# Performance work log

Hardware: AMD Instinct MI355X
Metric: run time of the kernel (lower is better)

## Reference

```python
import jax, jax.numpy as jnp
import numpy as np

N_NODES = 50000
N_EDGES = 800000
IN_CH, HID_CH, OUT_CH = 512, 128, 64


def gcn_conv(x, W, b, src, dst, num_nodes):
    """PyG GCNConv: add self-loops, sym-normalize, linear, scatter-add, bias.
    x: [N, Fin], W: [Fout, Fin], b: [Fout], src/dst: [E] int."""
    loop = jnp.arange(num_nodes, dtype=src.dtype)
    src2 = jnp.concatenate([src, loop])  # [E+N]
    dst2 = jnp.concatenate([dst, loop])
    deg = jax.ops.segment_sum(jnp.ones_like(dst2, dtype=x.dtype), dst2,
                              num_segments=num_nodes)  # in-degree + 1
    d_inv_sqrt = jnp.where(deg > 0, jax.lax.rsqrt(deg), 0.0)
    norm = d_inv_sqrt[src2] * d_inv_sqrt[dst2]  # [E+N]
    h = x @ W.T  # [N, Fout]
    msg = h[src2] * norm[:, None]  # [E+N, Fout] -- dominant memory traffic
    out = jax.ops.segment_sum(msg, dst2, num_segments=num_nodes)
    return out + b


def setup_inputs() -> dict:
    key = jax.random.key(0)
    ks = jax.random.split(key, 8)
    x = jax.random.normal(ks[0], (N_NODES, IN_CH), dtype=jnp.float32)
    edge_index = jax.random.randint(ks[1], (2, N_EDGES), 0, N_NODES, dtype=jnp.int64)
    s1 = 1.0 / np.sqrt(IN_CH)
    s2 = 1.0 / np.sqrt(HID_CH)
    W1 = jax.random.normal(ks[2], (HID_CH, IN_CH), dtype=jnp.float32) * s1
    b1 = jnp.zeros((HID_CH,), dtype=jnp.float32)
    W_mu = jax.random.normal(ks[3], (OUT_CH, HID_CH), dtype=jnp.float32) * s2
    b_mu = jnp.zeros((OUT_CH,), dtype=jnp.float32)
    W_logstd = jax.random.normal(ks[4], (OUT_CH, HID_CH), dtype=jnp.float32) * s2
    b_logstd = jnp.zeros((OUT_CH,), dtype=jnp.float32)
    return {"x": x, "edge_index": edge_index, "W1": W1, "b1": b1,
            "W_mu": W_mu, "b_mu": b_mu, "W_logstd": W_logstd, "b_logstd": b_logstd}


def reference(x, edge_index, W1, b1, W_mu, b_mu, W_logstd, b_logstd):
    src, dst = edge_index[0], edge_index[1]
    n = x.shape[0]
    h = jax.nn.relu(gcn_conv(x, W1, b1, src, dst, n))
    mu = gcn_conv(h, W_mu, b_mu, src, dst, n)
    logstd = gcn_conv(h, W_logstd, b_logstd, src, dst, n)
    return (mu, logstd)
```

## Files before the change

### kernel.cpp

```cpp
#include <hip/hip_runtime.h>

constexpr int FIN = 512;
constexpr int FH  = 128;
constexpr int FO  = 64;

typedef short short8 __attribute__((ext_vector_type(8)));
typedef float f32x4 __attribute__((ext_vector_type(4)));

__device__ __forceinline__ unsigned short f2bf(float f) {
    unsigned u = __float_as_uint(f);
    u += 0x7fffu + ((u >> 16) & 1u);
    return (unsigned short)(u >> 16);
}
__device__ __forceinline__ float bf2f(unsigned short h) {
    return __uint_as_float((unsigned)h << 16);
}
__device__ __forceinline__ float bflo(unsigned v) { return __uint_as_float(v << 16); }
__device__ __forceinline__ float bfhi(unsigned v) { return __uint_as_float(v & 0xffff0000u); }


__global__ void pre_kernel(const int* __restrict__ dst, int* __restrict__ cnt, int E,
                           const float* __restrict__ W1, unsigned short* __restrict__ W1b,
                           const float* __restrict__ Wmu, const float* __restrict__ Wlg,
                           unsigned short* __restrict__ Wh, unsigned short* __restrict__ Wl,
                           int cntB) {
    int b = blockIdx.x;
    if (b < cntB) {
        int i = b * 256 + threadIdx.x;
        if (i < E) atomicAdd(&cnt[dst[i]], 1);
    } else if (b < cntB + 64) {
        int i = (b - cntB) * 256 + threadIdx.x;
        float4 v = ((const float4*)W1)[i];
        ushort4 p;
        p.x = f2bf(v.x); p.y = f2bf(v.y); p.z = f2bf(v.z); p.w = f2bf(v.w);
        ((ushort4*)W1b)[i] = p;
    } else {
        int i = (b - cntB - 64) * 256 + threadIdx.x;
        int r = i >> 7, c = i & 127;
        float f = (r < 64) ? Wmu[r * 128 + c] : Wlg[(r - 64) * 128 + c];
        unsigned short h = f2bf(f);
        Wh[i] = h;
        Wl[i] = f2bf(f - bf2f(h));
    }
}


__global__ void scan1_kernel(const int* __restrict__ cnt, int* __restrict__ offs,
                             int* __restrict__ bsum, float* __restrict__ dinv, int n) {
    __shared__ int sdata[256];
    int t = threadIdx.x;
    int base = blockIdx.x * 1024 + t * 4;
    int4 c = make_int4(0, 0, 0, 0);
    if (base + 3 < n) {
        c = *(const int4*)(cnt + base);
    } else {
        if (base + 0 < n) c.x = cnt[base + 0];
        if (base + 1 < n) c.y = cnt[base + 1];
        if (base + 2 < n) c.z = cnt[base + 2];
        if (base + 3 < n) c.w = cnt[base + 3];
    }
    if (base + 0 < n) dinv[base + 0] = rsqrtf((float)(c.x + 1));
    if (base + 1 < n) dinv[base + 1] = rsqrtf((float)(c.y + 1));
    if (base + 2 < n) dinv[base + 2] = rsqrtf((float)(c.z + 1));
    if (base + 3 < n) dinv[base + 3] = rsqrtf((float)(c.w + 1));

    int s0 = c.x + c.y + c.z + c.w;
    sdata[t] = s0;
    __syncthreads();
    for (int off = 1; off < 256; off <<= 1) {
        int v = (t >= off) ? sdata[t - off] : 0;
        __syncthreads();
        sdata[t] += v;
        __syncthreads();
    }
    int excl = sdata[t] - s0;
    if (t == 255) bsum[blockIdx.x] = sdata[255];
    if (base + 0 < n) offs[base + 0] = excl;
    if (base + 1 < n) offs[base + 1] = excl + c.x;
    if (base + 2 < n) offs[base + 2] = excl + c.x + c.y;
    if (base + 3 < n) offs[base + 3] = excl + c.x + c.y + c.z;
}

__global__ void scan2_kernel(int* __restrict__ bsum, int nb) {
    __shared__ int sdata[256];
    int t = threadIdx.x;
    int v = (t < nb) ? bsum[t] : 0;
    sdata[t] = v;
    __syncthreads();
    for (int off = 1; off < 256; off <<= 1) {
        int u = (t >= off) ? sdata[t - off] : 0;
        __syncthreads();
        sdata[t] += u;
        __syncthreads();
    }
    if (t < nb) bsum[t] = sdata[t] - v;
}

__global__ void scan3_kernel(int* __restrict__ offs, const int* __restrict__ bsum,
                             int n, int E) {
    int i = blockIdx.x * blockDim.x + threadIdx.x;
    if (i < n) offs[i] += bsum[i >> 10];
    if (i == 0) offs[n] = E;
}


__global__ void fill_kernel(const int* __restrict__ src, const int* __restrict__ dst,
                            const float* __restrict__ dinv, const int* __restrict__ offs,
                            int* __restrict__ cursor, int2* __restrict__ esort, int E) {
    int i = blockIdx.x * blockDim.x + threadIdx.x;
    if (i < E) {
        int s = src[i];
        int d = dst[i];
        int pos = offs[d] + atomicAdd(&cursor[d], 1);
        float w = dinv[s] * dinv[d];
        esort[pos] = make_int2(s, __float_as_int(w));
    }
}


__global__ void spmm_kernel(const unsigned int* __restrict__ hin, const int* __restrict__ offs,
                            const int2* __restrict__ esort, const float* __restrict__ dinv,
                            const float* __restrict__ bias, unsigned int* __restrict__ hout,
                            int n, int relu) {
    int gid = blockIdx.x * blockDim.x + threadIdx.x;
    int node = gid >> 6;
    int lane = threadIdx.x & 63;
    if (node >= n) return;
    float di = dinv[node];
    unsigned hv = hin[(size_t)node * 64 + lane];
    float ax = di * di * bflo(hv);
    float ay = di * di * bfhi(hv);
    int p = offs[node];
    int end = offs[node + 1];
    if ((p & 1) && p < end) {
        int2 e = esort[p];
        unsigned v = hin[(size_t)e.x * 64 + lane];
        float w = __int_as_float(e.y);
        ax = fmaf(w, bflo(v), ax); ay = fmaf(w, bfhi(v), ay);
        ++p;
    }
    for (; p + 8 <= end; p += 8) {
        int4 q0 = *(const int4*)(esort + p + 0);
        int4 q1 = *(const int4*)(esort + p + 2);
        int4 q2 = *(const int4*)(esort + p + 4);
        int4 q3 = *(const int4*)(esort + p + 6);
        unsigned v0 = hin[(size_t)q0.x * 64 + lane];
        unsigned v1 = hin[(size_t)q0.z * 64 + lane];
        unsigned v2 = hin[(size_t)q1.x * 64 + lane];
        unsigned v3 = hin[(size_t)q1.z * 64 + lane];
        unsigned v4 = hin[(size_t)q2.x * 64 + lane];
        unsigned v5 = hin[(size_t)q2.z * 64 + lane];
        unsigned v6 = hin[(size_t)q3.x * 64 + lane];
        unsigned v7 = hin[(size_t)q3.z * 64 + lane];
        float w0 = __int_as_float(q0.y), w1 = __int_as_float(q0.w);
        float w2 = __int_as_float(q1.y), w3 = __int_as_float(q1.w);
        float w4 = __int_as_float(q2.y), w5 = __int_as_float(q2.w);
        float w6 = __int_as_float(q3.y), w7 = __int_as_float(q3.w);
        ax = fmaf(w0, bflo(v0), ax); ay = fmaf(w0, bfhi(v0), ay);
        ax = fmaf(w1, bflo(v1), ax); ay = fmaf(w1, bfhi(v1), ay);
        ax = fmaf(w2, bflo(v2), ax); ay = fmaf(w2, bfhi(v2), ay);
        ax = fmaf(w3, bflo(v3), ax); ay = fmaf(w3, bfhi(v3), ay);
        ax = fmaf(w4, bflo(v4), ax); ay = fmaf(w4, bfhi(v4), ay);
        ax = fmaf(w5, bflo(v5), ax); ay = fmaf(w5, bfhi(v5), ay);
        ax = fmaf(w6, bflo(v6), ax); ay = fmaf(w6, bfhi(v6), ay);
        ax = fmaf(w7, bflo(v7), ax); ay = fmaf(w7, bfhi(v7), ay);
    }
    for (; p + 2 <= end; p += 2) {
        int4 q = *(const int4*)(esort + p);
        unsigned v0 = hin[(size_t)q.x * 64 + lane];
        unsigned v1 = hin[(size_t)q.z * 64 + lane];
        float w0 = __int_as_float(q.y), w1 = __int_as_float(q.w);
        ax = fmaf(w0, bflo(v0), ax); ay = fmaf(w0, bfhi(v0), ay);
        ax = fmaf(w1, bflo(v1), ax); ay = fmaf(w1, bfhi(v1), ay);
    }
    if (p < end) {
        int2 e = esort[p];
        unsigned v = hin[(size_t)e.x * 64 + lane];
        float w = __int_as_float(e.y);
        ax = fmaf(w, bflo(v), ax); ay = fmaf(w, bfhi(v), ay);
    }
    if (bias) {
        float2 b = ((const float2*)bias)[lane];
        ax += b.x; ay += b.y;
    }
    if (relu) { ax = fmaxf(ax, 0.f); ay = fmaxf(ay, 0.f); }
    unsigned o = (unsigned)f2bf(ax) | ((unsigned)f2bf(ay) << 16);
    hout[(size_t)node * 64 + lane] = o;
}


__global__ __launch_bounds__(1024, 4) void gemm1_kernel(
    const float* __restrict__ X, const unsigned short* __restrict__ Wb,
    unsigned short* __restrict__ out, int M, int nstrips) {
    extern __shared__ __align__(16) unsigned short Bs[];
    int tid = threadIdx.x;

    #pragma unroll
    for (int j = 0; j < 8; ++j) {
        int f = tid + j * 1024;
        int row = f >> 6;
        unsigned addr = ((unsigned)f << 4) ^ ((unsigned)(row & 7) << 4);
        *(short8*)((char*)Bs + addr) = ((const short8*)Wb)[f];
    }
    __syncthreads();

    int lane = tid & 63, wid = tid >> 6;
    int fr = lane & 15, fq = lane >> 4;
    int s = wid * gridDim.x + blockIdx.x;
    if (s >= nstrips) return;
    int row0 = s * 16;
    int arow = row0 + fr; if (arow >= M) arow = M - 1;
    const float* ap = X + (size_t)arow * FIN + fq * 8;

    f32x4 acc[8] = {};

    float4 c0 = *(const float4*)(ap + 0);
    float4 c1 = *(const float4*)(ap + 4);
    float4 c2 = *(const float4*)(ap + 32);
    float4 c3 = *(const float4*)(ap + 36);

    #pragma unroll
    for (int kk = 0; kk < 8; ++kk) {
        int k0 = kk * 64;
        float4 d0 = c0, d1 = c1, d2 = c2, d3 = c3;
        if (kk < 7) {
            c0 = *(const float4*)(ap + k0 + 64);
            c1 = *(const float4*)(ap + k0 + 68);
            c2 = *(const float4*)(ap + k0 + 96);
            c3 = *(const float4*)(ap + k0 + 100);
        }
        short8 af0, af1;
        af0[0] = (short)f2bf(d0.x); af0[1] = (short)f2bf(d0.y);
        af0[2] = (short)f2bf(d0.z); af0[3] = (short)f2bf(d0.w);
        af0[4] = (short)f2bf(d1.x); af0[5] = (short)f2bf(d1.y);
        af0[6] = (short)f2bf(d1.z); af0[7] = (short)f2bf(d1.w);
        af1[0] = (short)f2bf(d2.x); af1[1] = (short)f2bf(d2.y);
        af1[2] = (short)f2bf(d2.z); af1[3] = (short)f2bf(d2.w);
        af1[4] = (short)f2bf(d3.x); af1[5] = (short)f2bf(d3.y);
        af1[6] = (short)f2bf(d3.z); af1[7] = (short)f2bf(d3.w);

        int cb0 = k0 * 2 + fq * 16;
        #pragma unroll
        for (int c = 0; c < 8; ++c) {
            int br = c * 16 + fr;
            short8 b0 = *(const short8*)((const char*)Bs + br * 1024 +
                                         ((unsigned)cb0 ^ ((unsigned)(br & 7) << 4)));
            acc[c] = __builtin_amdgcn_mfma_f32_16x16x32_bf16(af0, b0, acc[c], 0, 0, 0);
        }
        int cb1 = cb0 + 64;
        #pragma unroll
        for (int c = 0; c < 8; ++c) {
            int br = c * 16 + fr;
            short8 b1 = *(const short8*)((const char*)Bs + br * 1024 +
                                         ((unsigned)cb1 ^ ((unsigned)(br & 7) << 4)));
            acc[c] = __builtin_amdgcn_mfma_f32_16x16x32_bf16(af1, b1, acc[c], 0, 0, 0);
        }
    }

    #pragma unroll
    for (int c = 0; c < 8; ++c) {
        #pragma unroll
        for (int j = 0; j < 4; ++j) {
            int row = row0 + fq * 4 + j;
            if (row < M) out[(size_t)row * FH + c * 16 + fr] = f2bf(acc[c][j]);
        }
    }
}


__global__ __launch_bounds__(512) void gemm2_kernel(
    const unsigned short* __restrict__ Xb,
    const unsigned short* __restrict__ Wh, const unsigned short* __restrict__ Wl,
    float* __restrict__ outA, float* __restrict__ outB,
    const float* __restrict__ biasA, const float* __restrict__ biasB,
    int M, int nstrips) {
    __shared__ __align__(16) unsigned short WhS[128 * 128];
    __shared__ __align__(16) unsigned short WlS[128 * 128];
    int tid = threadIdx.x;

    #pragma unroll
    for (int j = 0; j < 4; ++j) {
        int f = tid + j * 512;
        int row = f >> 4;
        unsigned addr = ((unsigned)f * 16u) ^ ((unsigned)(row & 7) << 4);
        *(short8*)((char*)WhS + addr) = ((const short8*)Wh)[f];
        *(short8*)((char*)WlS + addr) = ((const short8*)Wl)[f];
    }
    __syncthreads();

    int lane = tid & 63, wid = tid >> 6;
    int fr = lane & 15, fq = lane >> 4;
    int s = blockIdx.x * 8 + wid;
    if (s >= nstrips) return;
    int row0 = s * 16;
    int arow = row0 + fr; if (arow > M - 1) arow = M - 1;
    const unsigned short* ap = Xb + (size_t)arow * FH + fq * 8;

    short8 a0 = *(const short8*)(ap + 0);
    short8 a1 = *(const short8*)(ap + 32);
    short8 a2 = *(const short8*)(ap + 64);
    short8 a3 = *(const short8*)(ap + 96);

    f32x4 acc[8] = {};

    auto proc = [&](int k0, short8 a) {
        int cb = k0 * 2 + fq * 16;
        #pragma unroll
        for (int c = 0; c < 8; ++c) {
            int lr = c * 16 + fr;
            unsigned addr = ((unsigned)(lr * 256 + cb)) ^ ((unsigned)(lr & 7) << 4);
            short8 bh = *(const short8*)((const char*)WhS + addr);
            short8 bl = *(const short8*)((const char*)WlS + addr);
            acc[c] = __builtin_amdgcn_mfma_f32_16x16x32_bf16(a, bh, acc[c], 0, 0, 0);
            acc[c] = __builtin_amdgcn_mfma_f32_16x16x32_bf16(a, bl, acc[c], 0, 0, 0);
        }
    };
    proc(0, a0);
    proc(32, a1);
    proc(64, a2);
    proc(96, a3);

    #pragma unroll
    for (int c = 0; c < 8; ++c) {
        float* outp = (c < 4) ? outA : outB;
        const float* bp = (c < 4) ? biasA : biasB;
        int col = (c & 3) * 16 + fr;
        float bv = bp[col];
        #pragma unroll
        for (int j = 0; j < 4; ++j) {
            int row = row0 + fq * 4 + j;
            if (row < M) outp[(size_t)row * FO + col] = acc[c][j] + bv;
        }
    }
}


extern "C" void kernel_launch(void* const* d_in, const int* in_sizes, int n_in,
                              void* d_out, int out_size, void* d_ws, size_t ws_size,
                              hipStream_t stream) {
    const float* x   = (const float*)d_in[0];
    const int*   ei  = (const int*)d_in[1];
    const float* W1  = (const float*)d_in[2];
    const float* b1  = (const float*)d_in[3];
    const float* Wmu = (const float*)d_in[4];
    const float* bmu = (const float*)d_in[5];
    const float* Wlg = (const float*)d_in[6];
    const float* blg = (const float*)d_in[7];

    const int n = in_sizes[0] / FIN;
    const int E = in_sizes[1] / 2;
    const int* src = ei;
    const int* dst = ei + E;
    const int nstrips = (n + 15) / 16;

    char* ws = (char*)d_ws;
    size_t off = 0;
    auto alloc = [&](size_t bytes) -> void* {
        void* p = ws + off;
        off = (off + bytes + 255) & ~((size_t)255);
        return p;
    };
    int*   cnt    = (int*)  alloc((size_t)n * 4);
    int*   offs   = (int*)  alloc((size_t)(n + 1) * 4);
    int*   cursor = (int*)  alloc((size_t)n * 4);
    int*   bsum   = (int*)  alloc(1024);
    float* dinv   = (float*)alloc((size_t)n * 4);
    int2*  esort  = (int2*) alloc((size_t)E * 8);
    unsigned short* hbf  = (unsigned short*)alloc((size_t)n * FH * 2);
    unsigned short* h1bf = (unsigned short*)alloc((size_t)n * FH * 2);
    unsigned short* ah2b = (unsigned short*)alloc((size_t)n * FH * 2);
    unsigned short* W1b = (unsigned short*)alloc((size_t)FH * FIN * 2);
    unsigned short* W2h = (unsigned short*)alloc((size_t)FH * FH * 2);
    unsigned short* W2l = (unsigned short*)alloc((size_t)FH * FH * 2);

    hipMemsetAsync(cnt, 0, (size_t)n * 4, stream);
    hipMemsetAsync(cursor, 0, (size_t)n * 4, stream);

    int cntB = (E + 255) / 256;
    pre_kernel<<<cntB + 128, 256, 0, stream>>>(dst, cnt, E, W1, W1b, Wmu, Wlg, W2h, W2l, cntB);

    int nb = (n + 1023) / 1024;
    scan1_kernel<<<nb, 256, 0, stream>>>(cnt, offs, bsum, dinv, n);
    scan2_kernel<<<1, 256, 0, stream>>>(bsum, nb);
    scan3_kernel<<<(n + 255) / 256, 256, 0, stream>>>(offs, bsum, n, E);

    fill_kernel<<<(E + 255) / 256, 256, 0, stream>>>(src, dst, dinv, offs, cursor, esort, E);

    gemm1_kernel<<<256, 1024, 128 * 1024, stream>>>(x, W1b, hbf, n, nstrips);
    spmm_kernel<<<(n + 3) / 4, 256, 0, stream>>>(
        (const unsigned*)hbf, offs, esort, dinv, b1, (unsigned*)h1bf, n, 1);
    spmm_kernel<<<(n + 3) / 4, 256, 0, stream>>>(
        (const unsigned*)h1bf, offs, esort, dinv, nullptr, (unsigned*)ah2b, n, 0);
    float* outmu = (float*)d_out;
    float* outlg = outmu + (size_t)n * FO;
    gemm2_kernel<<<(nstrips + 7) / 8, 512, 0, stream>>>(
        ah2b, W2h, W2l, outmu, outlg, bmu, blg, n, nstrips);
}
```

Baseline: 197.0 us.

## Split SpMM feature columns across blocks and process four edges per wavefront

The SpMM kernel is restructured so each wavefront covers one node but only a 16-column quarter of its features. The four 16-lane groups each take a different edge, and partial sums are combined with cross-lane shuffles. Blocks are ordered so the four column-quarter blocks for the same node group run adjacently, which should keep gathered rows and the edge list hot in cache. This gives more parallelism and memory requests in flight per edge, at the cost of reading the edge list four times and giving up the wider unrolled int4 loads of the old loop.

```diff
diff --git a/kernel.cpp b/kernel.cpp
--- a/kernel.cpp
+++ b/kernel.cpp
@@ -122,70 +122,44 @@
                             const int2* __restrict__ esort, const float* __restrict__ dinv,
                             const float* __restrict__ bias, unsigned int* __restrict__ hout,
                             int n, int relu) {
-    int gid = blockIdx.x * blockDim.x + threadIdx.x;
-    int node = gid >> 6;
+    int blk = blockIdx.x;
+    int r = blk & 7;
+    int g = blk >> 3;
+    int q = r & 3;
+    int ngrp = g * 2 + (r >> 2);
+    int wid = threadIdx.x >> 6;
+    int node = ngrp * 4 + wid;
+    if (node >= n) return;
     int lane = threadIdx.x & 63;
-    if (node >= n) return;
-    float di = dinv[node];
-    unsigned hv = hin[(size_t)node * 64 + lane];
-    float ax = di * di * bflo(hv);
-    float ay = di * di * bfhi(hv);
-    int p = offs[node];
-    int end = offs[node + 1];
-    if ((p & 1) && p < end) {
-        int2 e = esort[p];
-        unsigned v = hin[(size_t)e.x * 64 + lane];
+    int eslot = lane >> 4, cl = lane & 15;
+    const unsigned* hq = hin + q * 16 + cl;
+
+    int p0 = offs[node], end = offs[node + 1];
+    float ax = 0.f, ay = 0.f;
+    for (int p = p0; p < end; p += 4) {
+        int pe = p + eslot;
+        int2 e = (pe < end) ? esort[pe] : make_int2(node, 0);
+        unsigned v = hq[(size_t)e.x * 64];
         float w = __int_as_float(e.y);
-        ax = fmaf(w, bflo(v), ax); ay = fmaf(w, bfhi(v), ay);
-        ++p;
-    }
-    for (; p + 8 <= end; p += 8) {
-        int4 q0 = *(const int4*)(esort + p + 0);
-        int4 q1 = *(const int4*)(esort + p + 2);
-        int4 q2 = *(const int4*)(esort + p + 4);
-        int4 q3 = *(const int4*)(esort + p + 6);
-        unsigned v0 = hin[(size_t)q0.x * 64 + lane];
-        unsigned v1 = hin[(size_t)q0.z * 64 + lane];
-        unsigned v2 = hin[(size_t)q1.x * 64 + lane];
-        unsigned v3 = hin[(size_t)q1.z * 64 + lane];
-        unsigned v4 = hin[(size_t)q2.x * 64 + lane];
-        unsigned v5 = hin[(size_t)q2.z * 64 + lane];
-        unsigned v6 = hin[(size_t)q3.x * 64 + lane];
-        unsigned v7 = hin[(size_t)q3.z * 64 + lane];
-        float w0 = __int_as_float(q0.y), w1 = __int_as_float(q0.w);
-        float w2 = __int_as_float(q1.y), w3 = __int_as_float(q1.w);
-        float w4 = __int_as_float(q2.y), w5 = __int_as_float(q2.w);
-        float w6 = __int_as_float(q3.y), w7 = __int_as_float(q3.w);
-        ax = fmaf(w0, bflo(v0), ax); ay = fmaf(w0, bfhi(v0), ay);
-        ax = fmaf(w1, bflo(v1), ax); ay = fmaf(w1, bfhi(v1), ay);
-        ax = fmaf(w2, bflo(v2), ax); ay = fmaf(w2, bfhi(v2), ay);
-        ax = fmaf(w3, bflo(v3), ax); ay = fmaf(w3, bfhi(v3), ay);
-        ax = fmaf(w4, bflo(v4), ax); ay = fmaf(w4, bfhi(v4), ay);
-        ax = fmaf(w5, bflo(v5), ax); ay = fmaf(w5, bfhi(v5), ay);
-        ax = fmaf(w6, bflo(v6), ax); ay = fmaf(w6, bfhi(v6), ay);
-        ax = fmaf(w7, bflo(v7), ax); ay = fmaf(w7, bfhi(v7), ay);
-    }
-    for (; p + 2 <= end; p += 2) {
-        int4 q = *(const int4*)(esort + p);
-        unsigned v0 = hin[(size_t)q.x * 64 + lane];
-        unsigned v1 = hin[(size_t)q.z * 64 + lane];
-        float w0 = __int_as_float(q.y), w1 = __int_as_float(q.w);
-        ax = fmaf(w0, bflo(v0), ax); ay = fmaf(w0, bfhi(v0), ay);
-        ax = fmaf(w1, bflo(v1), ax); ay = fmaf(w1, bfhi(v1), ay);
-    }
-    if (p < end) {
-        int2 e = esort[p];
-        unsigned v = hin[(size_t)e.x * 64 + lane];
-        float w = __int_as_float(e.y);
-        ax = fmaf(w, bflo(v), ax); ay = fmaf(w, bfhi(v), ay);
-    }
-    if (bias) {
-        float2 b = ((const float2*)bias)[lane];
-        ax += b.x; ay += b.y;
-    }
-    if (relu) { ax = fmaxf(ax, 0.f); ay = fmaxf(ay, 0.f); }
-    unsigned o = (unsigned)f2bf(ax) | ((unsigned)f2bf(ay) << 16);
-    hout[(size_t)node * 64 + lane] = o;
+        ax = fmaf(w, bflo(v), ax);
+        ay = fmaf(w, bfhi(v), ay);
+    }
+    ax += __shfl_xor(ax, 16); ay += __shfl_xor(ay, 16);
+    ax += __shfl_xor(ax, 32); ay += __shfl_xor(ay, 32);
+
+    if (eslot == 0) {
+        float di = dinv[node];
+        unsigned hv = hq[(size_t)node * 64];
+        ax = fmaf(di * di, bflo(hv), ax);
+        ay = fmaf(di * di, bfhi(hv), ay);
+        if (bias) {
+            float2 b = ((const float2*)bias)[q * 16 + cl];
+            ax += b.x; ay += b.y;
+        }
+        if (relu) { ax = fmaxf(ax, 0.f); ay = fmaxf(ay, 0.f); }
+        unsigned o = (unsigned)f2bf(ax) | ((unsigned)f2bf(ay) << 16);
+        hout[(size_t)node * 64 + q * 16 + cl] = o;
+    }
 }
 
 
@@ -387,9 +361,12 @@
     fill_kernel<<<(E + 255) / 256, 256, 0, stream>>>(src, dst, dinv, offs, cursor, esort, E);
 
     gemm1_kernel<<<256, 1024, 128 * 1024, stream>>>(x, W1b, hbf, n, nstrips);
-    spmm_kernel<<<(n + 3) / 4, 256, 0, stream>>>(
+
+    int ngrps = (n + 3) / 4;
+    int gblocks = (ngrps + 1) / 2;
+    spmm_kernel<<<gblocks * 8, 256, 0, stream>>>(
         (const unsigned*)hbf, offs, esort, dinv, b1, (unsigned*)h1bf, n, 1);
-    spmm_kernel<<<(n + 3) / 4, 256, 0, stream>>>(
+    spmm_kernel<<<gblocks * 8, 256, 0, stream>>>(
         (const unsigned*)h1bf, offs, esort, dinv, nullptr, (unsigned*)ah2b, n, 0);
     float* outmu = (float*)d_out;
     float* outlg = outmu + (size_t)n * FO;
```

Result: slower. 352.0 us (+78.7%).
